# Performance work log

Measured on AMD Instinct MI355X. Metric: run time of the kernel, lower is better.

## Reference

```python
import jax, jax.numpy as jnp
import numpy as np

P, NT = 4, 524288
DZ = 1.0e-3     # z step (m)
DT = 0.01       # time step (ps)
GAMMA = 1.0e-3  # nonlinear coefficient
FR = 0.18       # Raman fraction
OMEGA0 = 1830.0 # carrier angular frequency (rad/ps), ~1030 nm


def setup_inputs() -> dict:
    key = jax.random.key(0)
    ks = jax.random.split(key, 7)
    A_re = jax.random.normal(ks[0], (P, NT), jnp.float32) * 0.5
    A_im = jax.random.normal(ks[1], (P, NT), jnp.float32) * 0.5
    S = jax.random.uniform(ks[2], (P, P, P, P), jnp.float32) * 0.1  # mode overlap tensor
    D_re = jax.random.normal(ks[3], (P, NT), jnp.float32) * 0.1
    D_im = jax.random.normal(ks[4], (P, NT), jnp.float32) * 0.01
    hrw_re = jax.random.normal(ks[5], (NT,), jnp.float32)
    hrw_im = jax.random.normal(ks[6], (NT,), jnp.float32)
    omega = (2.0 * np.pi * np.fft.fftfreq(NT, DT)).astype(np.float32)
    return {"A_re": A_re, "A_im": A_im, "S": S, "D_re": D_re, "D_im": D_im,
            "hrw_re": hrw_re, "hrw_im": hrw_im, "omega": jnp.asarray(omega), "nz": 10}


def _propagate(A0, S, D, hrw, omega, nz):
    # half-step linear (dispersion) phase, applied in the frequency domain
    lin = jnp.exp(0.5j * DZ * D)                       # (P, Nt)
    # self-steepening spectral prefactor  i*gamma*(1 + Omega/omega0)
    pref = (1j * GAMMA) * (1.0 + omega / OMEGA0)       # (Nt,)
    hrw_c = jnp.conj(hrw)                              # (Nt,)

    def nl(A):  # dA/dz from Kerr + Raman + self-steepening, A: (P, Nt) time domain
        S_kerr = jnp.einsum('pqrs,qt,rt,st->pt', S, A, A, jnp.conj(A))
        T = A[:, None, :] * jnp.conj(A)[None, :, :]    # (P, P, Nt)
        T_conv = jnp.fft.ifft(jnp.fft.fft(T, axis=-1) * hrw_c, axis=-1) * DT
        Vpl = jnp.einsum('pmrs,rst->pmt', S, T_conv)   # (P, P, Nt)
        S_raman = jnp.einsum('pmt,mt->pt', Vpl, A)     # (P, Nt)
        S_total = (1.0 - FR) * S_kerr + FR * S_raman
        return jnp.fft.fft(pref * jnp.fft.ifft(S_total, axis=-1), axis=-1)

    def step(carry, _):
        f, fw = carry
        fw = fw * lin
        f = jnp.fft.fft(fw, axis=-1)
        # RK4 for the nonlinear sub-step
        k1 = DZ * nl(f)
        k2 = DZ * nl(f + 0.5 * k1)
        k3 = DZ * nl(f + 0.5 * k2)
        k4 = DZ * nl(f + k3)
        f = f + (k1 + 2.0 * k2 + 2.0 * k3 + k4) / 6.0
        fw = jnp.fft.ifft(f, axis=-1) * lin
        return (f, fw), None

    fw0 = jnp.fft.ifft(A0, axis=-1)
    (f, fw), _ = jax.lax.scan(step, (A0, fw0), None, length=nz)
    return jnp.fft.fft(fw, axis=-1)


def reference(A_re, A_im, S, D_re, D_im, hrw_re, hrw_im, omega, nz):
    A = (A_re + 1j * A_im).astype(jnp.complex64)
    D = (D_re + 1j * D_im).astype(jnp.complex64)
    hrw = (hrw_re + 1j * hrw_im).astype(jnp.complex64)
    out = _propagate(A, S, D, hrw, omega, nz)          # (P, Nt) complex64
    return jnp.stack([out.real, out.imag])             # (2, P, Nt) float32
```

## Files before the change

### kernel.cpp

```cpp
#include <hip/hip_runtime.h>
#include <math.h>

#define NTOT (1 << 19)
#define NN1 512
#define NN2 1024
#define PM 4
#define NZ_STEPS 10

static const float DZv = 1.0e-3f;
static const float DTv = 0.01f;
static const float GAMMAv = 1.0e-3f;
static const float FRv = 0.18f;
static const float OMEGA0v = 1830.0f;

typedef float2 cplx;
__device__ inline cplx cmul(cplx a, cplx b) { return make_float2(a.x * b.x - a.y * b.y, a.x * b.y + a.y * b.x); }
__device__ inline cplx cadd(cplx a, cplx b) { return make_float2(a.x + b.x, a.y + b.y); }
__device__ inline cplx csub(cplx a, cplx b) { return make_float2(a.x - b.x, a.y - b.y); }
__device__ inline cplx cscale(cplx a, float s) { return make_float2(a.x * s, a.y * s); }
__device__ inline cplx conjc(cplx a) { return make_float2(a.x, -a.y); }
__device__ inline cplx expi_pi(float a, float sgn) {
    float s, c;
    sincospif(a, &s, &c);
    return make_float2(c, sgn * s);
}
__device__ inline int dig4rev10(int j) {
    return ((j & 3) << 8) | (((j >> 2) & 3) << 6) | (((j >> 4) & 3) << 4) | (((j >> 6) & 3) << 2) | ((j >> 8) & 3);
}
__device__ inline int b4rev8(int t) {
    return ((t & 3) << 6) | (((t >> 2) & 3) << 4) | (((t >> 4) & 3) << 2) | ((t >> 6) & 3);
}
__device__ inline int islot_512(int k1) { return ((k1 & 1) << 8) | b4rev8(k1 >> 1); }

#define SK(q) ((q) + ((q) >> 4))

#define TW_SZ 596
#define TWOFF(L) ((L) == 4 ? 0 : (L) == 16 ? 4 : (L) == 64 ? 20 : 84)
#define TWR2 340
__device__ inline void init_tw(cplx* tw, int tid) {
    for (int idx = tid; idx < TW_SZ; idx += 256) {
        float a;
        if (idx < 4) a = (float)idx * (0.5f / 4.0f);
        else if (idx < 20) a = (float)(idx - 4) * (0.5f / 16.0f);
        else if (idx < 84) a = (float)(idx - 20) * (0.5f / 64.0f);
        else if (idx < 340) a = (float)(idx - 84) * (0.5f / 256.0f);
        else a = (float)(idx - 340) * (1.0f / 256.0f);
        float s, c;
        sincospif(a, &s, &c);
        tw[idx] = make_float2(c, s);
    }
}
__device__ inline cplx twget(const cplx* tw, int off, int b, float SGN) {
    cplx t = tw[off + b];
    return make_float2(t.x, SGN * t.y);
}

__device__ inline void r4dif_w(cplx& x0, cplx& x1, cplx& x2, cplx& x3, cplx w1, float SGN) {
    cplx t0 = cadd(x0, x2), t1 = cadd(x1, x3), t2 = csub(x0, x2), t3 = csub(x1, x3);
    cplx ct3 = make_float2(-SGN * t3.y, SGN * t3.x);
    cplx w2 = cmul(w1, w1), w3 = cmul(w2, w1);
    x0 = cadd(t0, t1);
    x1 = cmul(cadd(t2, ct3), w1);
    x2 = cmul(csub(t0, t1), w2);
    x3 = cmul(csub(t2, ct3), w3);
}
__device__ inline void r4dif0(cplx& x0, cplx& x1, cplx& x2, cplx& x3, float SGN) {
    cplx t0 = cadd(x0, x2), t1 = cadd(x1, x3), t2 = csub(x0, x2), t3 = csub(x1, x3);
    cplx ct3 = make_float2(-SGN * t3.y, SGN * t3.x);
    x0 = cadd(t0, t1); x1 = cadd(t2, ct3); x2 = csub(t0, t1); x3 = csub(t2, ct3);
}
__device__ inline void r4dit_w(cplx& x0, cplx& x1, cplx& x2, cplx& x3, cplx w1, float SGN) {
    cplx w2 = cmul(w1, w1), w3 = cmul(w2, w1);
    cplx z1 = cmul(x1, w1), z2 = cmul(x2, w2), z3 = cmul(x3, w3);
    cplx t0 = cadd(x0, z2), t1 = cadd(z1, z3), t2 = csub(x0, z2), t3 = csub(z1, z3);
    cplx ct3 = make_float2(-SGN * t3.y, SGN * t3.x);
    x0 = cadd(t0, t1); x1 = cadd(t2, ct3); x2 = csub(t0, t1); x3 = csub(t2, ct3);
}
__device__ inline void r4dit0(cplx& x0, cplx& x1, cplx& x2, cplx& x3, float SGN) {
    cplx t0 = cadd(x0, x2), t1 = cadd(x1, x3), t2 = csub(x0, x2), t3 = csub(x1, x3);
    cplx ct3 = make_float2(-SGN * t3.y, SGN * t3.x);
    x0 = cadd(t0, t1); x1 = cadd(t2, ct3); x2 = csub(t0, t1); x3 = csub(t2, ct3);
}

template <bool INV, bool TFORM>
__global__ __launch_bounds__(256) void kA1(const cplx* __restrict__ in, cplx* __restrict__ out, int pair0) {
    __shared__ cplx ld[1024 + 64];
    __shared__ cplx tw[TW_SZ];
    const float SGN = INV ? 1.0f : -1.0f;
    int row = blockIdx.y;
    int n1 = blockIdx.x;
    int tid = threadIdx.x;
    const cplx* srcA;
    const cplx* srcB = nullptr;
    if (TFORM) {
        int rs = pair0 + row;
        srcA = in + (size_t)(rs >> 2) * NTOT;
        srcB = in + (size_t)(rs & 3) * NTOT;
    } else {
        srcA = in + (size_t)row * NTOT;
    }
    cplx* dst = out + (size_t)row * NTOT;
    size_t base = (size_t)n1 * NN2;
    cplx x0, x1, x2, x3;
    if (TFORM) {
        x0 = cmul(srcA[base + tid], conjc(srcB[base + tid]));
        x1 = cmul(srcA[base + tid + 256], conjc(srcB[base + tid + 256]));
        x2 = cmul(srcA[base + tid + 512], conjc(srcB[base + tid + 512]));
        x3 = cmul(srcA[base + tid + 768], conjc(srcB[base + tid + 768]));
    } else {
        x0 = srcA[base + tid];
        x1 = srcA[base + tid + 256];
        x2 = srcA[base + tid + 512];
        x3 = srcA[base + tid + 768];
    }
    init_tw(tw, tid);
    __syncthreads();
    r4dif_w(x0, x1, x2, x3, twget(tw, 84, tid, SGN), SGN);
    ld[SK(tid)] = x0; ld[SK(tid + 256)] = x1; ld[SK(tid + 512)] = x2; ld[SK(tid + 768)] = x3;
    __syncthreads();
    #pragma unroll
    for (int L = 64; L >= 4; L >>= 2) {
        int b = tid & (L - 1), g = tid / L;
        int p0 = g * 4 * L + b;
        cplx y0 = ld[SK(p0)], y1 = ld[SK(p0 + L)], y2 = ld[SK(p0 + 2 * L)], y3 = ld[SK(p0 + 3 * L)];
        r4dif_w(y0, y1, y2, y3, twget(tw, TWOFF(L), b, SGN), SGN);
        ld[SK(p0)] = y0; ld[SK(p0 + L)] = y1; ld[SK(p0 + 2 * L)] = y2; ld[SK(p0 + 3 * L)] = y3;
        __syncthreads();
    }
    {
        int p0 = 4 * tid;
        cplx y0 = ld[SK(p0)], y1 = ld[SK(p0 + 1)], y2 = ld[SK(p0 + 2)], y3 = ld[SK(p0 + 3)];
        r4dif0(y0, y1, y2, y3, SGN);
        int c = dig4rev10(p0);
        cplx w = expi_pi((float)(n1 * c) * (2.0f / (float)NTOT), SGN);
        if (INV) w = cscale(w, 1.0f / (float)NTOT);
        cplx dlt = expi_pi((float)n1 * (1.0f / 1024.0f), SGN);
        cplx o0 = cmul(y0, w);
        w = cmul(w, dlt);
        cplx o1 = cmul(y1, w);
        w = cmul(w, dlt);
        cplx o2 = cmul(y2, w);
        w = cmul(w, dlt);
        cplx o3 = cmul(y3, w);
        float4* d4 = (float4*)(dst + base + p0);
        d4[0] = make_float4(o0.x, o0.y, o1.x, o1.y);
        d4[1] = make_float4(o2.x, o2.y, o3.x, o3.y);
    }
}

#define APPLY_CT(o, n1v)                                                        \
    {                                                                           \
        cplx W0 = expi_pi((float)((n1v) * k2b) * (2.0f / (float)NTOT), SGN_B);  \
        if (CONV) W0 = cscale(W0, 1.0f / (float)NTOT);                          \
        cplx P1 = expi_pi((float)(n1v) * (1.0f / 1024.0f), SGN_B);              \
        cplx P2 = expi_pi((float)(n1v) * (1.0f / 4096.0f), SGN_B);              \
        cplx wct = W0;                                                          \
        o[0] = cmul(o[0], wct);                                                 \
        wct = cmul(wct, P1); o[1] = cmul(o[1], wct);                            \
        wct = cmul(wct, P1); o[2] = cmul(o[2], wct);                            \
        wct = cmul(wct, P1); o[3] = cmul(o[3], wct);                            \
        wct = cmul(W0, P2);  o[4] = cmul(o[4], wct);                            \
        wct = cmul(wct, P1); o[5] = cmul(o[5], wct);                            \
        wct = cmul(wct, P1); o[6] = cmul(o[6], wct);                            \
        wct = cmul(wct, P1); o[7] = cmul(o[7], wct);                            \
    }

template <bool CONV, int TMODE>
__global__ __launch_bounds__(256) void kM(const cplx* in, cplx* out, const cplx* __restrict__ tab) {
    __shared__ cplx ld[8 * 545];
    __shared__ cplx tw[TW_SZ];
    const float SGN_F = CONV ? -1.0f : 1.0f;
    const float SGN_B = -SGN_F;
    int row = blockIdx.y;
    int jb = blockIdx.x * 8;
    const cplx* src = in + (size_t)row * NTOT;
    cplx* dst = out + (size_t)row * NTOT;
    const cplx* trow = (TMODE == 3) ? tab : tab + (size_t)row * NTOT;
    int tid = threadIdx.x;
    int jj = tid & 7, n10 = tid >> 3;
    cplx v[16];
    #pragma unroll
    for (int m = 0; m < 16; m++) v[m] = src[(size_t)(n10 + 32 * m) * NN2 + jb + jj];
    init_tw(tw, tid);
    __syncthreads();
    #pragma unroll
    for (int m = 0; m < 8; m++) {
        int b = n10 + 32 * m;
        cplx u = v[m], w = v[m + 8];
        v[m] = cadd(u, w);
        v[m + 8] = cmul(csub(u, w), twget(tw, TWR2, b, SGN_F));
    }
    #pragma unroll
    for (int m = 0; m < 8; m++) {
        int b = n10 + 32 * m;
        ld[jj * 545 + SK(b)] = v[m];
        ld[jj * 545 + SK(b + 256)] = v[m + 8];
    }
    __syncthreads();
    #pragma unroll
    for (int L = 64; L >= 4; L >>= 2) {
        #pragma unroll
        for (int it = 0; it < 4; it++) {
            int gbf = it * 256 + tid;
            int r = gbf >> 7, rr = gbf & 127;
            int h = rr >> 6, s = rr & 63;
            int b = s & (L - 1), g = s / L;
            int q0 = h * 256 + g * 4 * L + b;
            cplx* rp = ld + r * 545;
            cplx y0 = rp[SK(q0)], y1 = rp[SK(q0 + L)], y2 = rp[SK(q0 + 2 * L)], y3 = rp[SK(q0 + 3 * L)];
            r4dif_w(y0, y1, y2, y3, twget(tw, TWOFF(L), b, SGN_F), SGN_F);
            rp[SK(q0)] = y0; rp[SK(q0 + L)] = y1; rp[SK(q0 + 2 * L)] = y2; rp[SK(q0 + 3 * L)] = y3;
        }
        __syncthreads();
    }
    #pragma unroll
    for (int it = 0; it < 4; it++) {
        int gbf = it * 256 + tid;
        int r = gbf >> 7, rr = gbf & 127;
        int h = rr >> 6, s = rr & 63;
        int q0 = h * 256 + 4 * s;
        cplx* rp = ld + r * 545;
        cplx y0 = rp[SK(q0)], y1 = rp[SK(q0 + 1)], y2 = rp[SK(q0 + 2)], y3 = rp[SK(q0 + 3)];
        r4dif0(y0, y1, y2, y3, SGN_F);
        size_t tb = (size_t)(jb + r) * NN1 + q0;
        const cplx* tp = trow + tb;
        cplx t0 = tp[0], t1 = tp[1], t2 = tp[2], t3 = tp[3];
        if (TMODE == 2) { t0 = cmul(t0, t0); t1 = cmul(t1, t1); t2 = cmul(t2, t2); t3 = cmul(t3, t3); }
        y0 = cmul(y0, t0); y1 = cmul(y1, t1); y2 = cmul(y2, t2); y3 = cmul(y3, t3);
        r4dit0(y0, y1, y2, y3, SGN_B);
        rp[SK(q0)] = y0; rp[SK(q0 + 1)] = y1; rp[SK(q0 + 2)] = y2; rp[SK(q0 + 3)] = y3;
    }
    __syncthreads();
    #pragma unroll
    for (int L = 4; L <= 64; L <<= 2) {
        #pragma unroll
        for (int it = 0; it < 4; it++) {
            int gbf = it * 256 + tid;
            int r = gbf >> 7, rr = gbf & 127;
            int h = rr >> 6, s = rr & 63;
            int b = s & (L - 1), g = s / L;
            int q0 = h * 256 + g * 4 * L + b;
            cplx* rp = ld + r * 545;
            cplx y0 = rp[SK(q0)], y1 = rp[SK(q0 + L)], y2 = rp[SK(q0 + 2 * L)], y3 = rp[SK(q0 + 3 * L)];
            r4dit_w(y0, y1, y2, y3, twget(tw, TWOFF(L), b, SGN_B), SGN_B);
            rp[SK(q0)] = y0; rp[SK(q0 + L)] = y1; rp[SK(q0 + 2 * L)] = y2; rp[SK(q0 + 3 * L)] = y3;
        }
        __syncthreads();
    }
    {
        int t = tid;
        cplx r2 = twget(tw, TWR2, t, SGN_B);
        cplx oa[8], ob[8];
        #pragma unroll
        for (int f = 0; f < 8; f++) {
            cplx u = ld[f * 545 + SK(t)];
            cplx w = ld[f * 545 + SK(t + 256)];
            cplx wv = cmul(w, r2);
            oa[f] = cadd(u, wv);
            ob[f] = csub(u, wv);
        }
        int k2b = dig4rev10(jb);
        APPLY_CT(oa, t);
        APPLY_CT(ob, t + 256);
        float4* da = (float4*)(dst + (size_t)t * NN2 + jb);
        da[0] = make_float4(oa[0].x, oa[0].y, oa[1].x, oa[1].y);
        da[1] = make_float4(oa[2].x, oa[2].y, oa[3].x, oa[3].y);
        da[2] = make_float4(oa[4].x, oa[4].y, oa[5].x, oa[5].y);
        da[3] = make_float4(oa[6].x, oa[6].y, oa[7].x, oa[7].y);
        float4* db = (float4*)(dst + (size_t)(t + 256) * NN2 + jb);
        db[0] = make_float4(ob[0].x, ob[0].y, ob[1].x, ob[1].y);
        db[1] = make_float4(ob[2].x, ob[2].y, ob[3].x, ob[3].y);
        db[2] = make_float4(ob[4].x, ob[4].y, ob[5].x, ob[5].y);
        db[3] = make_float4(ob[6].x, ob[6].y, ob[7].x, ob[7].y);
    }
}

template <bool RKEPI>
__global__ __launch_bounds__(256) void kB2T(const cplx* __restrict__ in, cplx* __restrict__ out,
                                            cplx* __restrict__ fP, cplx* __restrict__ kaccP,
                                            cplx* __restrict__ AtmpP, int stage) {
    __shared__ cplx ld[1024 + 64];
    __shared__ cplx tw[TW_SZ];
    const float SGN = -1.0f;
    int row = blockIdx.y;
    int n1 = blockIdx.x;
    int tid = threadIdx.x;
    size_t base = (size_t)row * NTOT + (size_t)n1 * NN2;
    const float4* s4 = (const float4*)(in + base);
    float4 va = s4[2 * tid], vb = s4[2 * tid + 1];
    init_tw(tw, tid);
    cplx y0 = make_float2(va.x, va.y), y1 = make_float2(va.z, va.w);
    cplx y2 = make_float2(vb.x, vb.y), y3 = make_float2(vb.z, vb.w);
    r4dit0(y0, y1, y2, y3, SGN);
    int q0 = 4 * tid;
    ld[SK(q0)] = y0; ld[SK(q0 + 1)] = y1; ld[SK(q0 + 2)] = y2; ld[SK(q0 + 3)] = y3;
    __syncthreads();
    #pragma unroll
    for (int L = 4; L <= 64; L <<= 2) {
        int b = tid & (L - 1), g = tid / L;
        int p0 = g * 4 * L + b;
        cplx z0 = ld[SK(p0)], z1 = ld[SK(p0 + L)], z2 = ld[SK(p0 + 2 * L)], z3 = ld[SK(p0 + 3 * L)];
        r4dit_w(z0, z1, z2, z3, twget(tw, TWOFF(L), b, SGN), SGN);
        ld[SK(p0)] = z0; ld[SK(p0 + L)] = z1; ld[SK(p0 + 2 * L)] = z2; ld[SK(p0 + 3 * L)] = z3;
        __syncthreads();
    }
    {
        int b = tid;
        cplx z0 = ld[SK(b)], z1 = ld[SK(b + 256)], z2 = ld[SK(b + 512)], z3 = ld[SK(b + 768)];
        r4dit_w(z0, z1, z2, z3, twget(tw, 84, b, SGN), SGN);
        cplx ya[4] = {z0, z1, z2, z3};
        #pragma unroll
        for (int q = 0; q < 4; q++) {
            size_t off = base + b + q * 256;
            cplx v = ya[q];
            if (RKEPI) {
                if (stage == 1) {
                    kaccP[off] = v;
                    AtmpP[off] = cadd(fP[off], cscale(v, 0.5f));
                } else if (stage == 2) {
                    kaccP[off] = cadd(kaccP[off], cscale(v, 2.0f));
                    AtmpP[off] = cadd(fP[off], cscale(v, 0.5f));
                } else if (stage == 3) {
                    kaccP[off] = cadd(kaccP[off], cscale(v, 2.0f));
                    AtmpP[off] = cadd(fP[off], v);
                } else {
                    fP[off] = cadd(fP[off], cscale(cadd(kaccP[off], v), 1.0f / 6.0f));
                }
            } else {
                out[off] = v;
            }
        }
    }
}

template <int NR, bool KERR>
__global__ __launch_bounds__(256) void kB2R(const cplx* in, const cplx* __restrict__ A,
                                            const float* __restrict__ Sg, cplx* St, int pair0) {
    __shared__ cplx ld[1024 + 64];
    __shared__ cplx tw[TW_SZ];
    __shared__ float Ssh[256];
    const float SGN = 1.0f;
    int n1 = blockIdx.x;
    int tid = threadIdx.x;
    Ssh[tid] = Sg[tid];
    init_tw(tw, tid);
    size_t tb = (size_t)n1 * NN2 + tid;
    cplx am[4][4];
    #pragma unroll
    for (int m = 0; m < 4; m++)
        #pragma unroll
        for (int q = 0; q < 4; q++)
            am[m][q] = A[(size_t)m * NTOT + tb + q * 256];
    cplx acc[4][4];
    #pragma unroll
    for (int p = 0; p < 4; p++)
        #pragma unroll
        for (int q = 0; q < 4; q++) acc[p][q] = make_float2(0.f, 0.f);
    const float4* s4 = (const float4*)(in + (size_t)n1 * NN2);
    float4 va = s4[2 * tid], vb = s4[2 * tid + 1];
    for (int rowi = 0; rowi < NR; rowi++) {
        cplx y0 = make_float2(va.x, va.y), y1 = make_float2(va.z, va.w);
        cplx y2 = make_float2(vb.x, vb.y), y3 = make_float2(vb.z, vb.w);
        int nr = (rowi + 1 < NR) ? rowi + 1 : NR - 1;
        const float4* s4n = (const float4*)(in + (size_t)nr * NTOT + (size_t)n1 * NN2);
        va = s4n[2 * tid]; vb = s4n[2 * tid + 1];
        r4dit0(y0, y1, y2, y3, SGN);
        int q0 = 4 * tid;
        ld[SK(q0)] = y0; ld[SK(q0 + 1)] = y1; ld[SK(q0 + 2)] = y2; ld[SK(q0 + 3)] = y3;
        __syncthreads();
        #pragma unroll
        for (int L = 4; L <= 64; L <<= 2) {
            int b = tid & (L - 1), g = tid / L;
            int p0 = g * 4 * L + b;
            cplx z0 = ld[SK(p0)], z1 = ld[SK(p0 + L)], z2 = ld[SK(p0 + 2 * L)], z3 = ld[SK(p0 + 3 * L)];
            r4dit_w(z0, z1, z2, z3, twget(tw, TWOFF(L), b, SGN), SGN);
            ld[SK(p0)] = z0; ld[SK(p0 + L)] = z1; ld[SK(p0 + 2 * L)] = z2; ld[SK(p0 + 3 * L)] = z3;
            __syncthreads();
        }
        {
            int b = tid;
            cplx z0 = ld[SK(b)], z1 = ld[SK(b + 256)], z2 = ld[SK(b + 512)], z3 = ld[SK(b + 768)];
            r4dit_w(z0, z1, z2, z3, twget(tw, 84, b, SGN), SGN);
            cplx tc[4] = {z0, z1, z2, z3};
            int rs = pair0 + rowi, r = rs >> 2, s = rs & 3;
            #pragma unroll
            for (int p = 0; p < 4; p++) {
                float c0 = Ssh[((p * 4 + 0) * 4 + r) * 4 + s];
                float c1 = Ssh[((p * 4 + 1) * 4 + r) * 4 + s];
                float c2 = Ssh[((p * 4 + 2) * 4 + r) * 4 + s];
                float c3 = Ssh[((p * 4 + 3) * 4 + r) * 4 + s];
                #pragma unroll
                for (int q = 0; q < 4; q++) {
                    cplx c;
                    c.x = c0 * am[0][q].x + c1 * am[1][q].x + c2 * am[2][q].x + c3 * am[3][q].x;
                    c.y = c0 * am[0][q].y + c1 * am[1][q].y + c2 * am[2][q].y + c3 * am[3][q].y;
                    acc[p][q] = cadd(acc[p][q], cmul(c, tc[q]));
                }
            }
        }
        __syncthreads();
    }
    #pragma unroll
    for (int q = 0; q < 4; q++) {
        size_t off = tb + q * 256;
        if (KERR) {
            cplx pp[4][4];
            #pragma unroll
            for (int r = 0; r < 4; r++)
                #pragma unroll
                for (int s = 0; s < 4; s++) pp[r][s] = cmul(am[r][q], conjc(am[s][q]));
            #pragma unroll
            for (int p = 0; p < 4; p++) {
                cplx kc = make_float2(0.f, 0.f);
                #pragma unroll
                for (int m = 0; m < 4; m++) {
                    cplx g = make_float2(0.f, 0.f);
                    #pragma unroll
                    for (int r = 0; r < 4; r++)
                        #pragma unroll
                        for (int s = 0; s < 4; s++) {
                            float coef = Ssh[((p * 4 + m) * 4 + r) * 4 + s];
                            g.x += coef * pp[r][s].x;
                            g.y += coef * pp[r][s].y;
                        }
                    kc = cadd(kc, cmul(g, am[m][q]));
                }
                St[(size_t)p * NTOT + off] = cadd(cscale(kc, 1.0f - FRv), cscale(acc[p][q], FRv));
            }
        } else {
            #pragma unroll
            for (int p = 0; p < 4; p++) {
                size_t idx = (size_t)p * NTOT + off;
                St[idx] = cadd(St[idx], cscale(acc[p][q], FRv));
            }
        }
    }
}

__global__ __launch_bounds__(256) void k_tables(const float* __restrict__ D_re, const float* __restrict__ D_im,
                                                const float* __restrict__ hrw_re, const float* __restrict__ hrw_im,
                                                const float* __restrict__ omega,
                                                cplx* __restrict__ lin, cplx* __restrict__ pref, cplx* __restrict__ hrwc) {
    int k = blockIdx.x * 256 + threadIdx.x;
    if (k >= NTOT) return;
    int k2 = k & (NN2 - 1), k1 = k >> 10;
    int j = dig4rev10(k2), i = islot_512(k1);
    int s2 = j * NN1 + i;
    float om = omega[k];
    pref[s2] = make_float2(0.0f, GAMMAv * DZv * (1.0f + om / OMEGA0v));
    hrwc[s2] = make_float2(hrw_re[k] * DTv, -hrw_im[k] * DTv);
    for (int p = 0; p < PM; p++) {
        float dr = D_re[(size_t)p * NTOT + k], di = D_im[(size_t)p * NTOT + k];
        float amp = expf(-0.5f * DZv * di);
        float s, c;
        sincosf(0.5f * DZv * dr, &s, &c);
        lin[(size_t)p * NTOT + s2] = make_float2(amp * c, amp * s);
    }
}

__global__ void k_in(const float* __restrict__ Are, const float* __restrict__ Aim, cplx* __restrict__ f) {
    __shared__ cplx t[32][33];
    int p = blockIdx.z;
    int n1b = blockIdx.x * 32, n2b = blockIdx.y * 32;
    int tx = threadIdx.x, ty = threadIdx.y;
    const float* ar = Are + (size_t)p * NTOT;
    const float* ai = Aim + (size_t)p * NTOT;
    for (int yy = ty; yy < 32; yy += 8) {
        size_t idx = (size_t)(n2b + yy) * NN1 + (n1b + tx);
        t[yy][tx] = make_float2(ar[idx], ai[idx]);
    }
    __syncthreads();
    cplx* dst = f + (size_t)p * NTOT;
    for (int yy = ty; yy < 32; yy += 8) {
        dst[(size_t)(n1b + yy) * NN2 + (n2b + tx)] = t[tx][yy];
    }
}

__global__ void k_out(const cplx* __restrict__ fin, float* __restrict__ out) {
    __shared__ cplx t[32][33];
    int p = blockIdx.z;
    int n1b = blockIdx.x * 32, n2b = blockIdx.y * 32;
    int tx = threadIdx.x, ty = threadIdx.y;
    const cplx* src = fin + (size_t)p * NTOT;
    for (int yy = ty; yy < 32; yy += 8) {
        t[yy][tx] = src[(size_t)(n1b + yy) * NN2 + (n2b + tx)];
    }
    __syncthreads();
    float* outr = out + (size_t)p * NTOT;
    float* outi = out + (size_t)(PM + p) * NTOT;
    for (int yy = ty; yy < 32; yy += 8) {
        cplx v = t[tx][yy];
        size_t idx = (size_t)(n2b + yy) * NN1 + (n1b + tx);
        outr[idx] = v.x;
        outi[idx] = v.y;
    }
}

extern "C" void kernel_launch(void* const* d_in, const int* in_sizes, int n_in,
                              void* d_out, int out_size, void* d_ws, size_t ws_size,
                              hipStream_t stream) {
    const float* Are = (const float*)d_in[0];
    const float* Aim = (const float*)d_in[1];
    const float* S = (const float*)d_in[2];
    const float* Dre = (const float*)d_in[3];
    const float* Dim = (const float*)d_in[4];
    const float* hre = (const float*)d_in[5];
    const float* him = (const float*)d_in[6];
    const float* omega = (const float*)d_in[7];

    const size_t ROW = (size_t)NTOT;
    if (ws_size < 38ULL * ROW * sizeof(cplx)) return;
    cplx* f = (cplx*)d_ws;
    cplx* Atmp = f + 4 * ROW;
    cplx* kacc = Atmp + 4 * ROW;
    cplx* lin = kacc + 4 * ROW;
    cplx* pref = lin + 4 * ROW;
    cplx* hrwc = pref + 1 * ROW;
    cplx* Tb = hrwc + 1 * ROW;
    cplx* Z = Tb + 4 * ROW;
    cplx* St = Z;

    dim3 b256(256);
    dim3 gT(16, 32, 4), bT(32, 8);
    dim3 gPW1(NTOT / 256);

    k_tables<<<gPW1, b256, 0, stream>>>(Dre, Dim, hre, him, omega, lin, pref, hrwc);
    k_in<<<gT, bT, 0, stream>>>(Are, Aim, f);

    for (int step = 0; step < NZ_STEPS; step++) {
        kA1<true, false><<<dim3(512, 4), b256, 0, stream>>>(f, Z, 0);
        if (step == 0)
            kM<false, 1><<<dim3(128, 4), b256, 0, stream>>>(Z, Z, lin);
        else
            kM<false, 2><<<dim3(128, 4), b256, 0, stream>>>(Z, Z, lin);
        kB2T<false><<<dim3(512, 4), b256, 0, stream>>>(Z, f, nullptr, nullptr, nullptr, 0);
        for (int st = 1; st <= 4; st++) {
            const cplx* Aarg = (st == 1) ? f : Atmp;
            kA1<false, true><<<dim3(512, 16), b256, 0, stream>>>(Aarg, Z, 0);
            kM<true, 3><<<dim3(128, 16), b256, 0, stream>>>(Z, Z, hrwc);
            kB2R<16, true><<<dim3(512), b256, 0, stream>>>(Z, Aarg, S, St, 0);
            kA1<true, false><<<dim3(512, 4), b256, 0, stream>>>(St, Tb, 0);
            kM<false, 3><<<dim3(128, 4), b256, 0, stream>>>(Tb, Tb, pref);
            kB2T<true><<<dim3(512, 4), b256, 0, stream>>>(Tb, nullptr, f, kacc, Atmp, st);
        }
    }
    kA1<true, false><<<dim3(512, 4), b256, 0, stream>>>(f, Z, 0);
    kM<false, 1><<<dim3(128, 4), b256, 0, stream>>>(Z, Z, lin);
    kB2T<false><<<dim3(512, 4), b256, 0, stream>>>(Z, Atmp, nullptr, nullptr, nullptr, 0);
    k_out<<<gT, bT, 0, stream>>>(Atmp, (float*)d_out);
}
```

Before: 8.932 ms.

## Fuse FFT passes across RK stages into combined nonlinear and RK kernels

```diff
diff --git a/kernel.cpp b/kernel.cpp
--- a/kernel.cpp
+++ b/kernel.cpp
@@ -82,70 +82,87 @@
     x0 = cadd(t0, t1); x1 = cadd(t2, ct3); x2 = csub(t0, t1); x3 = csub(t2, ct3);
 }
 
-template <bool INV, bool TFORM>
-__global__ __launch_bounds__(256) void kA1(const cplx* __restrict__ in, cplx* __restrict__ out, int pair0) {
-    __shared__ cplx ld[1024 + 64];
-    __shared__ cplx tw[TW_SZ];
+template <int ISGN>
+__device__ inline void fft_j2n2(const cplx* gsrc, cplx* y, cplx* ld, const cplx* tw, int tid) {
+    const float SGN = (float)ISGN;
+    const float4* s4 = (const float4*)gsrc;
+    float4 va = s4[2 * tid], vb = s4[2 * tid + 1];
+    cplx y0 = make_float2(va.x, va.y), y1 = make_float2(va.z, va.w);
+    cplx y2 = make_float2(vb.x, vb.y), y3 = make_float2(vb.z, vb.w);
+    r4dit0(y0, y1, y2, y3, SGN);
+    int q0 = 4 * tid;
+    ld[SK(q0)] = y0; ld[SK(q0 + 1)] = y1; ld[SK(q0 + 2)] = y2; ld[SK(q0 + 3)] = y3;
+    __syncthreads();
+    #pragma unroll
+    for (int L = 4; L <= 64; L <<= 2) {
+        int b = tid & (L - 1), g = tid / L;
+        int p0 = g * 4 * L + b;
+        cplx z0 = ld[SK(p0)], z1 = ld[SK(p0 + L)], z2 = ld[SK(p0 + 2 * L)], z3 = ld[SK(p0 + 3 * L)];
+        r4dit_w(z0, z1, z2, z3, twget(tw, TWOFF(L), b, SGN), SGN);
+        ld[SK(p0)] = z0; ld[SK(p0 + L)] = z1; ld[SK(p0 + 2 * L)] = z2; ld[SK(p0 + 3 * L)] = z3;
+        __syncthreads();
+    }
+    {
+        int b = tid;
+        cplx z0 = ld[SK(b)], z1 = ld[SK(b + 256)], z2 = ld[SK(b + 512)], z3 = ld[SK(b + 768)];
+        r4dit_w(z0, z1, z2, z3, twget(tw, 84, b, SGN), SGN);
+        y[0] = z0; y[1] = z1; y[2] = z2; y[3] = z3;
+    }
+    __syncthreads();
+}
+
+template <bool INV>
+__device__ inline void fft_n22j(cplx* y, cplx* ld, const cplx* tw, int tid, int n1, cplx* gdst) {
     const float SGN = INV ? 1.0f : -1.0f;
-    int row = blockIdx.y;
-    int n1 = blockIdx.x;
-    int tid = threadIdx.x;
-    const cplx* srcA;
-    const cplx* srcB = nullptr;
-    if (TFORM) {
-        int rs = pair0 + row;
-        srcA = in + (size_t)(rs >> 2) * NTOT;
-        srcB = in + (size_t)(rs & 3) * NTOT;
-    } else {
-        srcA = in + (size_t)row * NTOT;
-    }
-    cplx* dst = out + (size_t)row * NTOT;
-    size_t base = (size_t)n1 * NN2;
-    cplx x0, x1, x2, x3;
-    if (TFORM) {
-        x0 = cmul(srcA[base + tid], conjc(srcB[base + tid]));
-        x1 = cmul(srcA[base + tid + 256], conjc(srcB[base + tid + 256]));
-        x2 = cmul(srcA[base + tid + 512], conjc(srcB[base + tid + 512]));
-        x3 = cmul(srcA[base + tid + 768], conjc(srcB[base + tid + 768]));
-    } else {
-        x0 = srcA[base + tid];
-        x1 = srcA[base + tid + 256];
-        x2 = srcA[base + tid + 512];
-        x3 = srcA[base + tid + 768];
-    }
-    init_tw(tw, tid);
-    __syncthreads();
-    r4dif_w(x0, x1, x2, x3, twget(tw, 84, tid, SGN), SGN);
-    ld[SK(tid)] = x0; ld[SK(tid + 256)] = x1; ld[SK(tid + 512)] = x2; ld[SK(tid + 768)] = x3;
+    r4dif_w(y[0], y[1], y[2], y[3], twget(tw, 84, tid, SGN), SGN);
+    ld[SK(tid)] = y[0]; ld[SK(tid + 256)] = y[1]; ld[SK(tid + 512)] = y[2]; ld[SK(tid + 768)] = y[3];
     __syncthreads();
     #pragma unroll
     for (int L = 64; L >= 4; L >>= 2) {
         int b = tid & (L - 1), g = tid / L;
         int p0 = g * 4 * L + b;
-        cplx y0 = ld[SK(p0)], y1 = ld[SK(p0 + L)], y2 = ld[SK(p0 + 2 * L)], y3 = ld[SK(p0 + 3 * L)];
-        r4dif_w(y0, y1, y2, y3, twget(tw, TWOFF(L), b, SGN), SGN);
-        ld[SK(p0)] = y0; ld[SK(p0 + L)] = y1; ld[SK(p0 + 2 * L)] = y2; ld[SK(p0 + 3 * L)] = y3;
+        cplx z0 = ld[SK(p0)], z1 = ld[SK(p0 + L)], z2 = ld[SK(p0 + 2 * L)], z3 = ld[SK(p0 + 3 * L)];
+        r4dif_w(z0, z1, z2, z3, twget(tw, TWOFF(L), b, SGN), SGN);
+        ld[SK(p0)] = z0; ld[SK(p0 + L)] = z1; ld[SK(p0 + 2 * L)] = z2; ld[SK(p0 + 3 * L)] = z3;
         __syncthreads();
     }
     {
         int p0 = 4 * tid;
-        cplx y0 = ld[SK(p0)], y1 = ld[SK(p0 + 1)], y2 = ld[SK(p0 + 2)], y3 = ld[SK(p0 + 3)];
-        r4dif0(y0, y1, y2, y3, SGN);
+        cplx z0 = ld[SK(p0)], z1 = ld[SK(p0 + 1)], z2 = ld[SK(p0 + 2)], z3 = ld[SK(p0 + 3)];
+        r4dif0(z0, z1, z2, z3, SGN);
         int c = dig4rev10(p0);
         cplx w = expi_pi((float)(n1 * c) * (2.0f / (float)NTOT), SGN);
         if (INV) w = cscale(w, 1.0f / (float)NTOT);
         cplx dlt = expi_pi((float)n1 * (1.0f / 1024.0f), SGN);
-        cplx o0 = cmul(y0, w);
-        w = cmul(w, dlt);
-        cplx o1 = cmul(y1, w);
-        w = cmul(w, dlt);
-        cplx o2 = cmul(y2, w);
-        w = cmul(w, dlt);
-        cplx o3 = cmul(y3, w);
-        float4* d4 = (float4*)(dst + base + p0);
+        cplx o0 = cmul(z0, w); w = cmul(w, dlt);
+        cplx o1 = cmul(z1, w); w = cmul(w, dlt);
+        cplx o2 = cmul(z2, w); w = cmul(w, dlt);
+        cplx o3 = cmul(z3, w);
+        float4* d4 = (float4*)(gdst + p0);
         d4[0] = make_float4(o0.x, o0.y, o1.x, o1.y);
         d4[1] = make_float4(o2.x, o2.y, o3.x, o3.y);
     }
+    __syncthreads();
+}
+
+template <bool INV>
+__global__ __launch_bounds__(256) void kA1(const cplx* __restrict__ in, cplx* __restrict__ out) {
+    __shared__ cplx ld[1024 + 64];
+    __shared__ cplx tw[TW_SZ];
+    int row = blockIdx.y;
+    int n1 = blockIdx.x;
+    int tid = threadIdx.x;
+    const cplx* src = in + (size_t)row * NTOT;
+    cplx* dst = out + (size_t)row * NTOT;
+    size_t base = (size_t)n1 * NN2;
+    cplx y[4];
+    y[0] = src[base + tid];
+    y[1] = src[base + tid + 256];
+    y[2] = src[base + tid + 512];
+    y[3] = src[base + tid + 768];
+    init_tw(tw, tid);
+    __syncthreads();
+    fft_n22j<INV>(y, ld, tw, tid, n1, dst + base);
 }
 
 #define APPLY_CT(o, n1v)                                                        \
@@ -275,165 +292,171 @@
     }
 }
 
-template <bool RKEPI>
-__global__ __launch_bounds__(256) void kB2T(const cplx* __restrict__ in, cplx* __restrict__ out,
-                                            cplx* __restrict__ fP, cplx* __restrict__ kaccP,
-                                            cplx* __restrict__ AtmpP, int stage) {
+__global__ __launch_bounds__(256) void kB2T(const cplx* __restrict__ in, cplx* __restrict__ out) {
     __shared__ cplx ld[1024 + 64];
     __shared__ cplx tw[TW_SZ];
-    const float SGN = -1.0f;
     int row = blockIdx.y;
     int n1 = blockIdx.x;
     int tid = threadIdx.x;
     size_t base = (size_t)row * NTOT + (size_t)n1 * NN2;
-    const float4* s4 = (const float4*)(in + base);
-    float4 va = s4[2 * tid], vb = s4[2 * tid + 1];
     init_tw(tw, tid);
-    cplx y0 = make_float2(va.x, va.y), y1 = make_float2(va.z, va.w);
-    cplx y2 = make_float2(vb.x, vb.y), y3 = make_float2(vb.z, vb.w);
-    r4dit0(y0, y1, y2, y3, SGN);
-    int q0 = 4 * tid;
-    ld[SK(q0)] = y0; ld[SK(q0 + 1)] = y1; ld[SK(q0 + 2)] = y2; ld[SK(q0 + 3)] = y3;
-    __syncthreads();
-    #pragma unroll
-    for (int L = 4; L <= 64; L <<= 2) {
-        int b = tid & (L - 1), g = tid / L;
-        int p0 = g * 4 * L + b;
-        cplx z0 = ld[SK(p0)], z1 = ld[SK(p0 + L)], z2 = ld[SK(p0 + 2 * L)], z3 = ld[SK(p0 + 3 * L)];
-        r4dit_w(z0, z1, z2, z3, twget(tw, TWOFF(L), b, SGN), SGN);
-        ld[SK(p0)] = z0; ld[SK(p0 + L)] = z1; ld[SK(p0 + 2 * L)] = z2; ld[SK(p0 + 3 * L)] = z3;
-        __syncthreads();
-    }
-    {
-        int b = tid;
-        cplx z0 = ld[SK(b)], z1 = ld[SK(b + 256)], z2 = ld[SK(b + 512)], z3 = ld[SK(b + 768)];
-        r4dit_w(z0, z1, z2, z3, twget(tw, 84, b, SGN), SGN);
-        cplx ya[4] = {z0, z1, z2, z3};
-        #pragma unroll
-        for (int q = 0; q < 4; q++) {
-            size_t off = base + b + q * 256;
-            cplx v = ya[q];
-            if (RKEPI) {
-                if (stage == 1) {
-                    kaccP[off] = v;
-                    AtmpP[off] = cadd(fP[off], cscale(v, 0.5f));
-                } else if (stage == 2) {
-                    kaccP[off] = cadd(kaccP[off], cscale(v, 2.0f));
-                    AtmpP[off] = cadd(fP[off], cscale(v, 0.5f));
-                } else if (stage == 3) {
-                    kaccP[off] = cadd(kaccP[off], cscale(v, 2.0f));
-                    AtmpP[off] = cadd(fP[off], v);
-                } else {
-                    fP[off] = cadd(fP[off], cscale(cadd(kaccP[off], v), 1.0f / 6.0f));
-                }
-            } else {
-                out[off] = v;
-            }
-        }
-    }
-}
-
-template <int NR, bool KERR>
-__global__ __launch_bounds__(256) void kB2R(const cplx* in, const cplx* __restrict__ A,
-                                            const float* __restrict__ Sg, cplx* St, int pair0) {
+    cplx y[4];
+    fft_j2n2<-1>(in + base, y, ld, tw, tid);
+    #pragma unroll
+    for (int q = 0; q < 4; q++) out[base + tid + q * 256] = y[q];
+}
+
+__global__ __launch_bounds__(256) void kNL(const cplx* __restrict__ Zin, const cplx* __restrict__ A,
+                                           const float* __restrict__ Sg, cplx* __restrict__ Tbout) {
     __shared__ cplx ld[1024 + 64];
     __shared__ cplx tw[TW_SZ];
     __shared__ float Ssh[256];
-    const float SGN = 1.0f;
-    int n1 = blockIdx.x;
-    int tid = threadIdx.x;
+    int n1 = blockIdx.x, tid = threadIdx.x;
     Ssh[tid] = Sg[tid];
     init_tw(tw, tid);
-    size_t tb = (size_t)n1 * NN2 + tid;
+    size_t base = (size_t)n1 * NN2;
+    size_t tb = base + tid;
     cplx am[4][4];
     #pragma unroll
     for (int m = 0; m < 4; m++)
         #pragma unroll
-        for (int q = 0; q < 4; q++)
-            am[m][q] = A[(size_t)m * NTOT + tb + q * 256];
+        for (int q = 0; q < 4; q++) am[m][q] = A[(size_t)m * NTOT + tb + q * 256];
     cplx acc[4][4];
     #pragma unroll
     for (int p = 0; p < 4; p++)
         #pragma unroll
         for (int q = 0; q < 4; q++) acc[p][q] = make_float2(0.f, 0.f);
-    const float4* s4 = (const float4*)(in + (size_t)n1 * NN2);
-    float4 va = s4[2 * tid], vb = s4[2 * tid + 1];
-    for (int rowi = 0; rowi < NR; rowi++) {
-        cplx y0 = make_float2(va.x, va.y), y1 = make_float2(va.z, va.w);
-        cplx y2 = make_float2(vb.x, vb.y), y3 = make_float2(vb.z, vb.w);
-        int nr = (rowi + 1 < NR) ? rowi + 1 : NR - 1;
-        const float4* s4n = (const float4*)(in + (size_t)nr * NTOT + (size_t)n1 * NN2);
-        va = s4n[2 * tid]; vb = s4n[2 * tid + 1];
-        r4dit0(y0, y1, y2, y3, SGN);
-        int q0 = 4 * tid;
-        ld[SK(q0)] = y0; ld[SK(q0 + 1)] = y1; ld[SK(q0 + 2)] = y2; ld[SK(q0 + 3)] = y3;
-        __syncthreads();
-        #pragma unroll
-        for (int L = 4; L <= 64; L <<= 2) {
-            int b = tid & (L - 1), g = tid / L;
-            int p0 = g * 4 * L + b;
-            cplx z0 = ld[SK(p0)], z1 = ld[SK(p0 + L)], z2 = ld[SK(p0 + 2 * L)], z3 = ld[SK(p0 + 3 * L)];
-            r4dit_w(z0, z1, z2, z3, twget(tw, TWOFF(L), b, SGN), SGN);
-            ld[SK(p0)] = z0; ld[SK(p0 + L)] = z1; ld[SK(p0 + 2 * L)] = z2; ld[SK(p0 + 3 * L)] = z3;
-            __syncthreads();
-        }
-        {
-            int b = tid;
-            cplx z0 = ld[SK(b)], z1 = ld[SK(b + 256)], z2 = ld[SK(b + 512)], z3 = ld[SK(b + 768)];
-            r4dit_w(z0, z1, z2, z3, twget(tw, 84, b, SGN), SGN);
-            cplx tc[4] = {z0, z1, z2, z3};
-            int rs = pair0 + rowi, r = rs >> 2, s = rs & 3;
+    for (int rowi = 0; rowi < 16; rowi++) {
+        cplx tc[4];
+        fft_j2n2<1>(Zin + (size_t)rowi * NTOT + base, tc, ld, tw, tid);
+        int r = rowi >> 2, s = rowi & 3;
+        #pragma unroll
+        for (int p = 0; p < 4; p++) {
+            float c0 = Ssh[((p * 4 + 0) * 4 + r) * 4 + s];
+            float c1 = Ssh[((p * 4 + 1) * 4 + r) * 4 + s];
+            float c2 = Ssh[((p * 4 + 2) * 4 + r) * 4 + s];
+            float c3 = Ssh[((p * 4 + 3) * 4 + r) * 4 + s];
             #pragma unroll
-            for (int p = 0; p < 4; p++) {
-                float c0 = Ssh[((p * 4 + 0) * 4 + r) * 4 + s];
-                float c1 = Ssh[((p * 4 + 1) * 4 + r) * 4 + s];
-                float c2 = Ssh[((p * 4 + 2) * 4 + r) * 4 + s];
-                float c3 = Ssh[((p * 4 + 3) * 4 + r) * 4 + s];
+            for (int q = 0; q < 4; q++) {
+                cplx c;
+                c.x = c0 * am[0][q].x + c1 * am[1][q].x + c2 * am[2][q].x + c3 * am[3][q].x;
+                c.y = c0 * am[0][q].y + c1 * am[1][q].y + c2 * am[2][q].y + c3 * am[3][q].y;
+                acc[p][q] = cadd(acc[p][q], cmul(c, tc[q]));
+            }
+        }
+    }
+    #pragma unroll
+    for (int q = 0; q < 4; q++) {
+        cplx pp[4][4];
+        #pragma unroll
+        for (int r = 0; r < 4; r++)
+            #pragma unroll
+            for (int s = 0; s < 4; s++) pp[r][s] = cmul(am[r][q], conjc(am[s][q]));
+        #pragma unroll
+        for (int p = 0; p < 4; p++) {
+            cplx kc = make_float2(0.f, 0.f);
+            #pragma unroll
+            for (int m = 0; m < 4; m++) {
+                cplx g = make_float2(0.f, 0.f);
                 #pragma unroll
-                for (int q = 0; q < 4; q++) {
-                    cplx c;
-                    c.x = c0 * am[0][q].x + c1 * am[1][q].x + c2 * am[2][q].x + c3 * am[3][q].x;
-                    c.y = c0 * am[0][q].y + c1 * am[1][q].y + c2 * am[2][q].y + c3 * am[3][q].y;
-                    acc[p][q] = cadd(acc[p][q], cmul(c, tc[q]));
-                }
+                for (int r = 0; r < 4; r++)
+                    #pragma unroll
+                    for (int s = 0; s < 4; s++) {
+                        float coef = Ssh[((p * 4 + m) * 4 + r) * 4 + s];
+                        g.x += coef * pp[r][s].x;
+                        g.y += coef * pp[r][s].y;
+                    }
+                kc = cadd(kc, cmul(g, am[m][q]));
             }
-        }
-        __syncthreads();
-    }
-    #pragma unroll
-    for (int q = 0; q < 4; q++) {
-        size_t off = tb + q * 256;
-        if (KERR) {
-            cplx pp[4][4];
+            acc[p][q] = cadd(cscale(kc, 1.0f - FRv), cscale(acc[p][q], FRv));
+        }
+    }
+    #pragma unroll
+    for (int p = 0; p < 4; p++) {
+        cplx y[4] = {acc[p][0], acc[p][1], acc[p][2], acc[p][3]};
+        fft_n22j<true>(y, ld, tw, tid, n1, Tbout + (size_t)p * NTOT + base);
+    }
+}
+
+template <int STAGE>
+__global__ __launch_bounds__(256) void kRK(const cplx* Tbin, const cplx* __restrict__ fP,
+                                           cplx* __restrict__ kaccP, cplx* __restrict__ AtmpP,
+                                           cplx* ZOut) {
+    __shared__ cplx ld[1024 + 64];
+    __shared__ cplx tw[TW_SZ];
+    int n1 = blockIdx.x, tid = threadIdx.x;
+    init_tw(tw, tid);
+    size_t base = (size_t)n1 * NN2;
+    cplx an[4][4];
+    #pragma unroll
+    for (int p = 0; p < 4; p++) {
+        cplx y[4];
+        fft_j2n2<-1>(Tbin + (size_t)p * NTOT + base, y, ld, tw, tid);
+        #pragma unroll
+        for (int q = 0; q < 4; q++) {
+            size_t off = (size_t)p * NTOT + base + tid + q * 256;
+            cplx v = y[q];
+            if (STAGE == 1) {
+                kaccP[off] = v;
+                an[p][q] = cadd(fP[off], cscale(v, 0.5f));
+                AtmpP[off] = an[p][q];
+            } else if (STAGE == 2) {
+                kaccP[off] = cadd(kaccP[off], cscale(v, 2.0f));
+                an[p][q] = cadd(fP[off], cscale(v, 0.5f));
+                AtmpP[off] = an[p][q];
+            } else if (STAGE == 3) {
+                kaccP[off] = cadd(kaccP[off], cscale(v, 2.0f));
+                an[p][q] = cadd(fP[off], v);
+                AtmpP[off] = an[p][q];
+            } else {
+                an[p][q] = cadd(fP[off], cscale(cadd(kaccP[off], v), 1.0f / 6.0f));
+            }
+        }
+    }
+    if (STAGE <= 3) {
+        #pragma unroll
+        for (int rs = 0; rs < 16; rs++) {
+            int r = rs >> 2, s = rs & 3;
+            cplx y[4];
             #pragma unroll
-            for (int r = 0; r < 4; r++)
-                #pragma unroll
-                for (int s = 0; s < 4; s++) pp[r][s] = cmul(am[r][q], conjc(am[s][q]));
-            #pragma unroll
-            for (int p = 0; p < 4; p++) {
-                cplx kc = make_float2(0.f, 0.f);
-                #pragma unroll
-                for (int m = 0; m < 4; m++) {
-                    cplx g = make_float2(0.f, 0.f);
-                    #pragma unroll
-                    for (int r = 0; r < 4; r++)
-                        #pragma unroll
-                        for (int s = 0; s < 4; s++) {
-                            float coef = Ssh[((p * 4 + m) * 4 + r) * 4 + s];
-                            g.x += coef * pp[r][s].x;
-                            g.y += coef * pp[r][s].y;
-                        }
-                    kc = cadd(kc, cmul(g, am[m][q]));
-                }
-                St[(size_t)p * NTOT + off] = cadd(cscale(kc, 1.0f - FRv), cscale(acc[p][q], FRv));
-            }
-        } else {
-            #pragma unroll
-            for (int p = 0; p < 4; p++) {
-                size_t idx = (size_t)p * NTOT + off;
-                St[idx] = cadd(St[idx], cscale(acc[p][q], FRv));
-            }
-        }
+            for (int q = 0; q < 4; q++) y[q] = cmul(an[r][q], conjc(an[s][q]));
+            fft_n22j<false>(y, ld, tw, tid, n1, ZOut + (size_t)rs * NTOT + base);
+        }
+    } else {
+        #pragma unroll
+        for (int p = 0; p < 4; p++) {
+            cplx y[4] = {an[p][0], an[p][1], an[p][2], an[p][3]};
+            fft_n22j<true>(y, ld, tw, tid, n1, ZOut + (size_t)p * NTOT + base);
+        }
+    }
+}
+
+__global__ __launch_bounds__(256) void kBD(const cplx* __restrict__ Tbin, cplx* __restrict__ fP,
+                                           cplx* __restrict__ ZOut) {
+    __shared__ cplx ld[1024 + 64];
+    __shared__ cplx tw[TW_SZ];
+    int n1 = blockIdx.x, tid = threadIdx.x;
+    init_tw(tw, tid);
+    size_t base = (size_t)n1 * NN2;
+    cplx an[4][4];
+    #pragma unroll
+    for (int p = 0; p < 4; p++) {
+        cplx y[4];
+        fft_j2n2<-1>(Tbin + (size_t)p * NTOT + base, y, ld, tw, tid);
+        #pragma unroll
+        for (int q = 0; q < 4; q++) {
+            size_t off = (size_t)p * NTOT + base + tid + q * 256;
+            an[p][q] = y[q];
+            fP[off] = y[q];
+        }
+    }
+    #pragma unroll
+    for (int rs = 0; rs < 16; rs++) {
+        int r = rs >> 2, s = rs & 3;
+        cplx y[4];
+        #pragma unroll
+        for (int q = 0; q < 4; q++) y[q] = cmul(an[r][q], conjc(an[s][q]));
+        fft_n22j<false>(y, ld, tw, tid, n1, ZOut + (size_t)rs * NTOT + base);
     }
 }
 
@@ -518,7 +541,6 @@
     cplx* hrwc = pref + 1 * ROW;
     cplx* Tb = hrwc + 1 * ROW;
     cplx* Z = Tb + 4 * ROW;
-    cplx* St = Z;
 
     dim3 b256(256);
     dim3 gT(16, 32, 4), bT(32, 8);
@@ -526,26 +548,30 @@
 
     k_tables<<<gPW1, b256, 0, stream>>>(Dre, Dim, hre, him, omega, lin, pref, hrwc);
     k_in<<<gT, bT, 0, stream>>>(Are, Aim, f);
+    kA1<true><<<dim3(512, 4), b256, 0, stream>>>(f, Tb);
 
     for (int step = 0; step < NZ_STEPS; step++) {
-        kA1<true, false><<<dim3(512, 4), b256, 0, stream>>>(f, Z, 0);
         if (step == 0)
-            kM<false, 1><<<dim3(128, 4), b256, 0, stream>>>(Z, Z, lin);
+            kM<false, 1><<<dim3(128, 4), b256, 0, stream>>>(Tb, Tb, lin);
         else
-            kM<false, 2><<<dim3(128, 4), b256, 0, stream>>>(Z, Z, lin);
-        kB2T<false><<<dim3(512, 4), b256, 0, stream>>>(Z, f, nullptr, nullptr, nullptr, 0);
+            kM<false, 2><<<dim3(128, 4), b256, 0, stream>>>(Tb, Tb, lin);
+        kBD<<<dim3(512), b256, 0, stream>>>(Tb, f, Z);
         for (int st = 1; st <= 4; st++) {
             const cplx* Aarg = (st == 1) ? f : Atmp;
-            kA1<false, true><<<dim3(512, 16), b256, 0, stream>>>(Aarg, Z, 0);
             kM<true, 3><<<dim3(128, 16), b256, 0, stream>>>(Z, Z, hrwc);
-            kB2R<16, true><<<dim3(512), b256, 0, stream>>>(Z, Aarg, S, St, 0);
-            kA1<true, false><<<dim3(512, 4), b256, 0, stream>>>(St, Tb, 0);
+            kNL<<<dim3(512), b256, 0, stream>>>(Z, Aarg, S, Tb);
             kM<false, 3><<<dim3(128, 4), b256, 0, stream>>>(Tb, Tb, pref);
-            kB2T<true><<<dim3(512, 4), b256, 0, stream>>>(Tb, nullptr, f, kacc, Atmp, st);
-        }
-    }
-    kA1<true, false><<<dim3(512, 4), b256, 0, stream>>>(f, Z, 0);
-    kM<false, 1><<<dim3(128, 4), b256, 0, stream>>>(Z, Z, lin);
-    kB2T<false><<<dim3(512, 4), b256, 0, stream>>>(Z, Atmp, nullptr, nullptr, nullptr, 0);
+            if (st == 1)
+                kRK<1><<<dim3(512), b256, 0, stream>>>(Tb, f, kacc, Atmp, Z);
+            else if (st == 2)
+                kRK<2><<<dim3(512), b256, 0, stream>>>(Tb, f, kacc, Atmp, Z);
+            else if (st == 3)
+                kRK<3><<<dim3(512), b256, 0, stream>>>(Tb, f, kacc, Atmp, Z);
+            else
+                kRK<4><<<dim3(512), b256, 0, stream>>>(Tb, f, kacc, nullptr, Tb);
+        }
+    }
+    kM<false, 1><<<dim3(128, 4), b256, 0, stream>>>(Tb, Tb, lin);
+    kB2T<<<dim3(512, 4), b256, 0, stream>>>(Tb, Atmp);
     k_out<<<gT, bT, 0, stream>>>(Atmp, (float*)d_out);
 }
```

Measured after the change: 8.797 ms. About the same (-1.5%).
